# Kernel optimization log

Hardware: AMD Instinct MI355X
Metric: run time of the kernel (lower is better)

## Reference

```python
import jax, jax.numpy as jnp
import numpy as np

BETA = 0.1
TRUNC = 1.0
MIN_VALID_RATIO = 0.3


def _wls_affine(x, y, w):
    # Weighted least squares fit of y ~ s*x + t over the last axis.
    sw = w.sum(-1)
    swx = (w * x).sum(-1)
    swy = (w * y).sum(-1)
    swxx = (w * x * x).sum(-1)
    swxy = (w * x * y).sum(-1)
    det = sw * swxx - swx * swx
    det = jnp.where(jnp.abs(det) < 1e-12, 1e-12, det)
    s = (sw * swxy - swx * swy) / det
    t = (swxx * swy - swx * swxy) / det
    return s, t


def _align_depth_affine(x, y, w, trunc):
    # Truncated robust affine alignment: initial WLS fit, then refit with
    # weights of points whose weighted residual exceeds `trunc` zeroed out
    # (falling back to the original weights if everything is truncated).
    s0, t0 = _wls_affine(x, y, w)
    e = w * jnp.abs(s0[..., None] * x + t0[..., None] - y)
    w2 = w * (e < trunc).astype(w.dtype)
    w2 = jnp.where(w2.sum(-1, keepdims=True) > 1e-8, w2, w)
    return _wls_affine(x, y, w2)


def _smooth(err, beta):
    if beta == 0:
        return err
    return jnp.where(err < beta, 0.5 * err * err / beta, err - 0.5 * beta)


def setup_inputs() -> dict:
    key = jax.random.key(0)
    k1, k2, k3 = jax.random.split(key, 3)
    B = 8
    P = 4096  # num_patches
    K = 256   # patch_pixel_count
    N = P * K
    pred_depth = jax.random.uniform(k1, (B, N), jnp.float32, 0.05, 5.0)
    gt_depth = jax.random.uniform(k2, (B, N), jnp.float32, 0.05, 5.0)
    mask = jax.random.bernoulli(k3, 0.8, (B, N))
    global_scale = jnp.ones((B,), jnp.float32)
    return {
        "pred_depth": pred_depth,
        "gt_depth": gt_depth,
        "mask": mask,
        "global_scale": global_scale,
        "num_patches": P,
        "patch_pixel_count": K,
    }


def reference(pred_depth, gt_depth, mask, global_scale, num_patches, patch_pixel_count):
    B = pred_depth.shape[0]
    P, K = num_patches, patch_pixel_count
    x = pred_depth.reshape(B, P, K)
    y = gt_depth.reshape(B, P, K)
    m = mask.reshape(B, P, K).astype(x.dtype)

    valid_ratio = m.mean(-1)                      # (B, P)
    msum = m.sum(-1)
    mean_depth = jnp.where(msum > 0, (y * m).sum(-1) / jnp.maximum(msum, 1.0), 1.0)

    w = m / jnp.maximum(y, 1e-5)                  # alignment weights (B, P, K)
    s, t = _align_depth_affine(x, y, w, TRUNC)    # (B, P) scale / shift per patch

    ratio = s / jnp.maximum(global_scale[:, None], 1e-12)
    gs_ok = jnp.where(global_scale[:, None] > 0, (ratio >= 0.1) & (ratio <= 10.0), True)
    valid = (valid_ratio >= MIN_VALID_RATIO) & (s > 0) & gs_ok  # (B, P)

    aligned = s[..., None] * x + t[..., None]
    pw = m / jnp.maximum(y, 0.1 * mean_depth[..., None])
    patch_loss = _smooth(jnp.abs(aligned - y) * pw, BETA).mean(-1)  # (B, P)

    vf = valid.astype(x.dtype)
    cnt = vf.sum()
    loss = jnp.where(cnt > 0, (patch_loss * vf).sum() / jnp.maximum(cnt, 1.0), 0.0)
    return loss
```

## Files before the change

kernel.cpp:

```cpp
#include <hip/hip_runtime.h>


#define WPB 4
#define NSLOTS 64
#define MAXBLK 2048

__device__ __forceinline__ float wredu(float v) {
#define DPP_ADD(ctrl)                                                        \
  v += __int_as_float(__builtin_amdgcn_update_dpp(                           \
      0, __float_as_int(v), (ctrl), 0xf, 0xf, true))
  DPP_ADD(0x111);
  DPP_ADD(0x112);
  DPP_ADD(0x114);
  DPP_ADD(0x118);
  DPP_ADD(0x142);
  DPP_ADD(0x143);
#undef DPP_ADD
  return __int_as_float(__builtin_amdgcn_readlane(__float_as_int(v), 63));
}

__device__ __forceinline__ float frcp(float x) {
  return __builtin_amdgcn_rcpf(x);
}

__global__ __launch_bounds__(256) void moge_patch_kernel(
    const float* __restrict__ xg,
    const float* __restrict__ yg,
    const int*   __restrict__ mg,
    const float* __restrict__ gsg,
    const int*   __restrict__ pP,
    const int*   __restrict__ pK,
    int B,
    float* __restrict__ ws) {
  const int P = pP[0];
  const int K = pK[0];
  const int lane = threadIdx.x & 63;
  const int wib  = threadIdx.x >> 6;
  const int total_patches = B * P;
  const int wave_stride = gridDim.x * WPB;
  const float invK = 1.0f / (float)K;

  float wloss = 0.f, wcnt = 0.f;

  if (K == 256) {
    int patch = blockIdx.x * WPB + wib;
    if (patch < total_patches) {
      const int loff = lane * 4;
      long base = (long)patch * 256 + loff;
      float4 x4 = *(const float4*)(xg + base);
      float4 y4 = *(const float4*)(yg + base);
      int4   m4 = *(const int4*)(mg + base);

      for (;;) {
        const int next = patch + wave_stride;
        const bool has_next = next < total_patches;
        const long nbase = (has_next ? (long)next * 256 : 0) + loff;
        const float4 nx4 = *(const float4*)(xg + nbase);
        const float4 ny4 = *(const float4*)(yg + nbase);
        const int4   nm4 = *(const int4*)(mg + nbase);

        float xr[4] = {x4.x, x4.y, x4.z, x4.w};
        float yr[4] = {y4.x, y4.y, y4.z, y4.w};
        float mr[4] = {m4.x ? 1.f : 0.f, m4.y ? 1.f : 0.f,
                       m4.z ? 1.f : 0.f, m4.w ? 1.f : 0.f};
        float wr[4];

        float sw = 0.f, swx = 0.f, swy = 0.f, swxx = 0.f, swxy = 0.f;
        float msum = 0.f, symsum = 0.f;
        #pragma unroll
        for (int i = 0; i < 4; ++i) {
          const float m = mr[i], xx = xr[i], yy = yr[i];
          const float w = m * frcp(fmaxf(yy, 1e-5f));
          wr[i] = w;
          const float wx = w * xx;
          sw += w; swx += wx; swy = fmaf(w, yy, swy);
          swxx = fmaf(wx, xx, swxx); swxy = fmaf(wx, yy, swxy);
          msum += m; symsum = fmaf(m, yy, symsum);
        }
        sw = wredu(sw); swx = wredu(swx); swy = wredu(swy);
        swxx = wredu(swxx); swxy = wredu(swxy);

        float det = sw * swxx - swx * swx;
        if (fabsf(det) < 1e-12f) det = 1e-12f;
        float rdet = frcp(det);
        const float s0 = (sw * swxy - swx * swy) * rdet;
        const float t0 = (swxx * swy - swx * swxy) * rdet;

        float sw2 = 0.f, swx2 = 0.f, swy2 = 0.f, swxx2 = 0.f, swxy2 = 0.f;
        #pragma unroll
        for (int i = 0; i < 4; ++i) {
          const float xx = xr[i], yy = yr[i], w = wr[i];
          const float e = w * fabsf(fmaf(s0, xx, t0) - yy);
          const float w2 = (e < 1.0f) ? w : 0.f;
          const float w2x = w2 * xx;
          sw2 += w2; swx2 += w2x; swy2 = fmaf(w2, yy, swy2);
          swxx2 = fmaf(w2x, xx, swxx2); swxy2 = fmaf(w2x, yy, swxy2);
        }
        sw2 = wredu(sw2); swx2 = wredu(swx2); swy2 = wredu(swy2);
        swxx2 = wredu(swxx2); swxy2 = wredu(swxy2);
        msum = wredu(msum); symsum = wredu(symsum);

        if (sw2 > 1e-8f) {
          sw = sw2; swx = swx2; swy = swy2; swxx = swxx2; swxy = swxy2;
        }
        det = sw * swxx - swx * swx;
        if (fabsf(det) < 1e-12f) det = 1e-12f;
        rdet = frcp(det);
        const float s = (sw * swxy - swx * swy) * rdet;
        const float t = (swxx * swy - swx * swxy) * rdet;

        const float mean_depth =
            (msum > 0.f) ? (symsum * frcp(fmaxf(msum, 1.f))) : 1.f;
        const float yfloor = 0.1f * mean_depth;

        float lsum = 0.f;
        #pragma unroll
        for (int i = 0; i < 4; ++i) {
          const float pw = mr[i] * frcp(fmaxf(yr[i], yfloor));
          const float err = fabsf(fmaf(s, xr[i], t) - yr[i]) * pw;
          lsum += (err < 0.1f) ? (5.0f * err * err) : (err - 0.05f);
        }
        const float patch_loss = wredu(lsum) * invK;

        const float gs = gsg[patch / P];
        const float ratio = s * frcp(fmaxf(gs, 1e-12f));
        const bool gs_ok = (gs > 0.f) ? (ratio >= 0.1f && ratio <= 10.0f) : true;
        const bool valid = (msum * invK >= 0.3f) && (s > 0.f) && gs_ok;

        if (valid) { wloss += patch_loss; wcnt += 1.f; }

        if (!has_next) break;
        patch = next; x4 = nx4; y4 = ny4; m4 = nm4;
      }
    }
  } else {
    for (int patch = blockIdx.x * WPB + wib; patch < total_patches;
         patch += wave_stride) {
      const long base = (long)patch * (long)K;
      const float* xp = xg + base;
      const float* yp = yg + base;
      const int*   mp = mg + base;

      float sw = 0.f, swx = 0.f, swy = 0.f, swxx = 0.f, swxy = 0.f;
      float msum = 0.f, symsum = 0.f;
      for (int j = lane; j < K; j += 64) {
        const float m = mp[j] ? 1.f : 0.f;
        const float xx = xp[j], yy = yp[j];
        const float w = m * frcp(fmaxf(yy, 1e-5f));
        const float wx = w * xx;
        sw += w; swx += wx; swy = fmaf(w, yy, swy);
        swxx = fmaf(wx, xx, swxx); swxy = fmaf(wx, yy, swxy);
        msum += m; symsum = fmaf(m, yy, symsum);
      }
      sw = wredu(sw); swx = wredu(swx); swy = wredu(swy);
      swxx = wredu(swxx); swxy = wredu(swxy);
      msum = wredu(msum); symsum = wredu(symsum);

      float det = sw * swxx - swx * swx;
      if (fabsf(det) < 1e-12f) det = 1e-12f;
      float rdet = frcp(det);
      const float s0 = (sw * swxy - swx * swy) * rdet;
      const float t0 = (swxx * swy - swx * swxy) * rdet;

      float sw2 = 0.f, swx2 = 0.f, swy2 = 0.f, swxx2 = 0.f, swxy2 = 0.f;
      for (int j = lane; j < K; j += 64) {
        const float m = mp[j] ? 1.f : 0.f;
        const float xx = xp[j], yy = yp[j];
        const float w = m * frcp(fmaxf(yy, 1e-5f));
        const float e = w * fabsf(fmaf(s0, xx, t0) - yy);
        const float w2 = (e < 1.0f) ? w : 0.f;
        const float w2x = w2 * xx;
        sw2 += w2; swx2 += w2x; swy2 = fmaf(w2, yy, swy2);
        swxx2 = fmaf(w2x, xx, swxx2); swxy2 = fmaf(w2x, yy, swxy2);
      }
      sw2 = wredu(sw2); swx2 = wredu(swx2); swy2 = wredu(swy2);
      swxx2 = wredu(swxx2); swxy2 = wredu(swxy2);

      if (sw2 > 1e-8f) {
        sw = sw2; swx = swx2; swy = swy2; swxx = swxx2; swxy = swxy2;
      }
      det = sw * swxx - swx * swx;
      if (fabsf(det) < 1e-12f) det = 1e-12f;
      rdet = frcp(det);
      const float s = (sw * swxy - swx * swy) * rdet;
      const float t = (swxx * swy - swx * swxy) * rdet;

      const float mean_depth =
          (msum > 0.f) ? (symsum * frcp(fmaxf(msum, 1.f))) : 1.f;
      const float yfloor = 0.1f * mean_depth;

      float lsum = 0.f;
      for (int j = lane; j < K; j += 64) {
        const float m = mp[j] ? 1.f : 0.f;
        const float xx = xp[j], yy = yp[j];
        const float pw = m * frcp(fmaxf(yy, yfloor));
        const float err = fabsf(fmaf(s, xx, t) - yy) * pw;
        lsum += (err < 0.1f) ? (5.0f * err * err) : (err - 0.05f);
      }
      const float patch_loss = wredu(lsum) * invK;

      const float gs = gsg[patch / P];
      const float ratio = s * frcp(fmaxf(gs, 1e-12f));
      const bool gs_ok = (gs > 0.f) ? (ratio >= 0.1f && ratio <= 10.0f) : true;
      const bool valid = (msum * invK >= 0.3f) && (s > 0.f) && gs_ok;

      if (valid) { wloss += patch_loss; wcnt += 1.f; }
    }
  }

  __shared__ float sl[WPB], sc[WPB];
  if (lane == 0) { sl[wib] = wloss; sc[wib] = wcnt; }
  __syncthreads();
  if (threadIdx.x == 0) {
    float bl = 0.f, bc = 0.f;
    #pragma unroll
    for (int i = 0; i < WPB; ++i) { bl += sl[i]; bc += sc[i]; }
    const int slot = (blockIdx.x & (NSLOTS - 1)) * 32;
    atomicAdd(&ws[slot], bl);
    atomicAdd(&ws[slot + 1], bc);
  }
}

__global__ void finalize_kernel(const float* __restrict__ ws,
                                float* __restrict__ out) {
  const int t = threadIdx.x;
  float l = wredu(ws[t * 32]);
  float c = wredu(ws[t * 32 + 1]);
  if (t == 0) out[0] = (c > 0.f) ? (l / fmaxf(c, 1.f)) : 0.f;
}

extern "C" void kernel_launch(void* const* d_in, const int* in_sizes, int n_in,
                              void* d_out, int out_size, void* d_ws, size_t ws_size,
                              hipStream_t stream) {
  const float* pred = (const float*)d_in[0];
  const float* gt   = (const float*)d_in[1];
  const int*   mask = (const int*)d_in[2];
  const float* gs   = (const float*)d_in[3];
  const int*   pP   = (const int*)d_in[4];
  const int*   pK   = (const int*)d_in[5];
  const int B = in_sizes[3];
  const long total_pixels = (long)in_sizes[0];
  float* ws = (float*)d_ws;

  hipMemsetAsync(ws, 0, NSLOTS * 32 * sizeof(float), stream);

  long est_patches = total_pixels / 256;
  long blocks = (est_patches + WPB - 1) / WPB;
  if (blocks < 1) blocks = 1;
  if (blocks > MAXBLK) blocks = MAXBLK;
  moge_patch_kernel<<<(int)blocks, 256, 0, stream>>>(pred, gt, mask, gs, pP,
                                                     pK, B, ws);
  finalize_kernel<<<1, 64, 0, stream>>>(ws, (float*)d_out);
}
```

Measured before the change: 128.9 us.

## Process four patches per wave with 16-lane row reductions

Each wavefront now handles four patches at once: every 16-lane DPP row owns one patch and each lane loads 16 contiguous pixels as four float4 loads per array. Wave-wide reductions become 4-step row reductions, which cuts the cross-lane shuffle work per patch. The launch uses a quarter as many blocks. The explicit software prefetch of the next patch is removed, so latency hiding now relies on more loads in flight per lane and on occupancy, and register use goes up from the 16-element arrays.

Measured after the change: 127.9 us. No clear change (-0.7%).

```diff
diff --git a/kernel.cpp b/kernel.cpp
--- a/kernel.cpp
+++ b/kernel.cpp
@@ -2,6 +2,7 @@
 
 
 #define WPB 4
+#define PPW 4
 #define NSLOTS 64
 #define MAXBLK 2048
 
@@ -17,6 +18,18 @@
   DPP_ADD(0x143);
 #undef DPP_ADD
   return __int_as_float(__builtin_amdgcn_readlane(__float_as_int(v), 63));
+}
+
+__device__ __forceinline__ float rowredu(float v) {
+#define DPP_ADD(ctrl)                                                        \
+  v += __int_as_float(__builtin_amdgcn_update_dpp(                           \
+      0, __float_as_int(v), (ctrl), 0xf, 0xf, true))
+  DPP_ADD(0x121);
+  DPP_ADD(0x122);
+  DPP_ADD(0x124);
+  DPP_ADD(0x128);
+#undef DPP_ADD
+  return v;
 }
 
 __device__ __forceinline__ float frcp(float x) {
@@ -37,103 +50,103 @@
   const int lane = threadIdx.x & 63;
   const int wib  = threadIdx.x >> 6;
   const int total_patches = B * P;
-  const int wave_stride = gridDim.x * WPB;
   const float invK = 1.0f / (float)K;
 
   float wloss = 0.f, wcnt = 0.f;
 
   if (K == 256) {
-    int patch = blockIdx.x * WPB + wib;
-    if (patch < total_patches) {
-      const int loff = lane * 4;
-      long base = (long)patch * 256 + loff;
-      float4 x4 = *(const float4*)(xg + base);
-      float4 y4 = *(const float4*)(yg + base);
-      int4   m4 = *(const int4*)(mg + base);
-
-      for (;;) {
-        const int next = patch + wave_stride;
-        const bool has_next = next < total_patches;
-        const long nbase = (has_next ? (long)next * 256 : 0) + loff;
-        const float4 nx4 = *(const float4*)(xg + nbase);
-        const float4 ny4 = *(const float4*)(yg + nbase);
-        const int4   nm4 = *(const int4*)(mg + nbase);
-
-        float xr[4] = {x4.x, x4.y, x4.z, x4.w};
-        float yr[4] = {y4.x, y4.y, y4.z, y4.w};
-        float mr[4] = {m4.x ? 1.f : 0.f, m4.y ? 1.f : 0.f,
-                       m4.z ? 1.f : 0.f, m4.w ? 1.f : 0.f};
-        float wr[4];
-
-        float sw = 0.f, swx = 0.f, swy = 0.f, swxx = 0.f, swxy = 0.f;
-        float msum = 0.f, symsum = 0.f;
-        #pragma unroll
-        for (int i = 0; i < 4; ++i) {
-          const float m = mr[i], xx = xr[i], yy = yr[i];
-          const float w = m * frcp(fmaxf(yy, 1e-5f));
-          wr[i] = w;
-          const float wx = w * xx;
-          sw += w; swx += wx; swy = fmaf(w, yy, swy);
-          swxx = fmaf(wx, xx, swxx); swxy = fmaf(wx, yy, swxy);
-          msum += m; symsum = fmaf(m, yy, symsum);
-        }
-        sw = wredu(sw); swx = wredu(swx); swy = wredu(swy);
-        swxx = wredu(swxx); swxy = wredu(swxy);
-
-        float det = sw * swxx - swx * swx;
-        if (fabsf(det) < 1e-12f) det = 1e-12f;
-        float rdet = frcp(det);
-        const float s0 = (sw * swxy - swx * swy) * rdet;
-        const float t0 = (swxx * swy - swx * swxy) * rdet;
-
-        float sw2 = 0.f, swx2 = 0.f, swy2 = 0.f, swxx2 = 0.f, swxy2 = 0.f;
-        #pragma unroll
-        for (int i = 0; i < 4; ++i) {
-          const float xx = xr[i], yy = yr[i], w = wr[i];
-          const float e = w * fabsf(fmaf(s0, xx, t0) - yy);
-          const float w2 = (e < 1.0f) ? w : 0.f;
-          const float w2x = w2 * xx;
-          sw2 += w2; swx2 += w2x; swy2 = fmaf(w2, yy, swy2);
-          swxx2 = fmaf(w2x, xx, swxx2); swxy2 = fmaf(w2x, yy, swxy2);
-        }
-        sw2 = wredu(sw2); swx2 = wredu(swx2); swy2 = wredu(swy2);
-        swxx2 = wredu(swxx2); swxy2 = wredu(swxy2);
-        msum = wredu(msum); symsum = wredu(symsum);
-
-        if (sw2 > 1e-8f) {
-          sw = sw2; swx = swx2; swy = swy2; swxx = swxx2; swxy = swxy2;
-        }
-        det = sw * swxx - swx * swx;
-        if (fabsf(det) < 1e-12f) det = 1e-12f;
-        rdet = frcp(det);
-        const float s = (sw * swxy - swx * swy) * rdet;
-        const float t = (swxx * swy - swx * swxy) * rdet;
-
-        const float mean_depth =
-            (msum > 0.f) ? (symsum * frcp(fmaxf(msum, 1.f))) : 1.f;
-        const float yfloor = 0.1f * mean_depth;
-
-        float lsum = 0.f;
-        #pragma unroll
-        for (int i = 0; i < 4; ++i) {
-          const float pw = mr[i] * frcp(fmaxf(yr[i], yfloor));
-          const float err = fabsf(fmaf(s, xr[i], t) - yr[i]) * pw;
-          lsum += (err < 0.1f) ? (5.0f * err * err) : (err - 0.05f);
-        }
-        const float patch_loss = wredu(lsum) * invK;
-
-        const float gs = gsg[patch / P];
-        const float ratio = s * frcp(fmaxf(gs, 1e-12f));
-        const bool gs_ok = (gs > 0.f) ? (ratio >= 0.1f && ratio <= 10.0f) : true;
-        const bool valid = (msum * invK >= 0.3f) && (s > 0.f) && gs_ok;
-
-        if (valid) { wloss += patch_loss; wcnt += 1.f; }
-
-        if (!has_next) break;
-        patch = next; x4 = nx4; y4 = ny4; m4 = nm4;
-      }
+    const int row = lane >> 4;
+    const int col = lane & 15;
+    const int poff = col * 16;
+    const int wave_stride = gridDim.x * WPB * PPW;
+
+    for (int pbase = (blockIdx.x * WPB + wib) * PPW; pbase < total_patches;
+         pbase += wave_stride) {
+      const int patch = pbase + row;
+      const bool row_ok = patch < total_patches;
+      const long base = (row_ok ? (long)patch * 256L : 0L) + poff;
+
+      float4 xa[4], ya[4]; int4 ma[4];
+      #pragma unroll
+      for (int j = 0; j < 4; ++j) {
+        xa[j] = *(const float4*)(xg + base + 4 * j);
+        ya[j] = *(const float4*)(yg + base + 4 * j);
+        ma[j] = *(const int4*)(mg + base + 4 * j);
+      }
+      const float* xr = (const float*)xa;
+      const float* yr = (const float*)ya;
+      const int*   mi = (const int*)ma;
+      float wv[16];
+
+      float sw = 0.f, swx = 0.f, swy = 0.f, swxx = 0.f, swxy = 0.f;
+      float msum = 0.f, symsum = 0.f;
+      #pragma unroll
+      for (int i = 0; i < 16; ++i) {
+        const float m = mi[i] ? 1.f : 0.f;
+        const float xx = xr[i], yy = yr[i];
+        const float w = m * frcp(fmaxf(yy, 1e-5f));
+        wv[i] = w;
+        const float wx = w * xx;
+        sw += w; swx += wx; swy = fmaf(w, yy, swy);
+        swxx = fmaf(wx, xx, swxx); swxy = fmaf(wx, yy, swxy);
+        msum += m; symsum = fmaf(m, yy, symsum);
+      }
+      sw = rowredu(sw); swx = rowredu(swx); swy = rowredu(swy);
+      swxx = rowredu(swxx); swxy = rowredu(swxy);
+
+      float det = sw * swxx - swx * swx;
+      if (fabsf(det) < 1e-12f) det = 1e-12f;
+      float rdet = frcp(det);
+      const float s0 = (sw * swxy - swx * swy) * rdet;
+      const float t0 = (swxx * swy - swx * swxy) * rdet;
+
+      float sw2 = 0.f, swx2 = 0.f, swy2 = 0.f, swxx2 = 0.f, swxy2 = 0.f;
+      #pragma unroll
+      for (int i = 0; i < 16; ++i) {
+        const float xx = xr[i], yy = yr[i], w = wv[i];
+        const float e = w * fabsf(fmaf(s0, xx, t0) - yy);
+        const float w2 = (e < 1.0f) ? w : 0.f;
+        const float w2x = w2 * xx;
+        sw2 += w2; swx2 += w2x; swy2 = fmaf(w2, yy, swy2);
+        swxx2 = fmaf(w2x, xx, swxx2); swxy2 = fmaf(w2x, yy, swxy2);
+      }
+      sw2 = rowredu(sw2); swx2 = rowredu(swx2); swy2 = rowredu(swy2);
+      swxx2 = rowredu(swxx2); swxy2 = rowredu(swxy2);
+      msum = rowredu(msum); symsum = rowredu(symsum);
+
+      if (sw2 > 1e-8f) {
+        sw = sw2; swx = swx2; swy = swy2; swxx = swxx2; swxy = swxy2;
+      }
+      det = sw * swxx - swx * swx;
+      if (fabsf(det) < 1e-12f) det = 1e-12f;
+      rdet = frcp(det);
+      const float s = (sw * swxy - swx * swy) * rdet;
+      const float t = (swxx * swy - swx * swxy) * rdet;
+
+      const float mean_depth =
+          (msum > 0.f) ? (symsum * frcp(fmaxf(msum, 1.f))) : 1.f;
+      const float yfloor = 0.1f * mean_depth;
+
+      float lsum = 0.f;
+      #pragma unroll
+      for (int i = 0; i < 16; ++i) {
+        const float m = (wv[i] > 0.f) ? 1.f : 0.f;
+        const float pw = m * frcp(fmaxf(yr[i], yfloor));
+        const float err = fabsf(fmaf(s, xr[i], t) - yr[i]) * pw;
+        lsum += (err < 0.1f) ? (5.0f * err * err) : (err - 0.05f);
+      }
+      const float patch_loss = rowredu(lsum) * invK;
+
+      const int pidx = row_ok ? patch : (total_patches - 1);
+      const float gs = gsg[(unsigned)pidx / (unsigned)P];
+      const float ratio = s * frcp(fmaxf(gs, 1e-12f));
+      const bool gs_ok = (gs > 0.f) ? (ratio >= 0.1f && ratio <= 10.0f) : true;
+      const bool valid = (msum * invK >= 0.3f) && (s > 0.f) && gs_ok;
+
+      if (col == 0 && row_ok && valid) { wloss += patch_loss; wcnt += 1.f; }
     }
   } else {
+    const int wave_stride = gridDim.x * WPB;
     for (int patch = blockIdx.x * WPB + wib; patch < total_patches;
          patch += wave_stride) {
       const long base = (long)patch * (long)K;
@@ -199,15 +212,17 @@
       }
       const float patch_loss = wredu(lsum) * invK;
 
-      const float gs = gsg[patch / P];
+      const float gs = gsg[(unsigned)patch / (unsigned)P];
       const float ratio = s * frcp(fmaxf(gs, 1e-12f));
       const bool gs_ok = (gs > 0.f) ? (ratio >= 0.1f && ratio <= 10.0f) : true;
       const bool valid = (msum * invK >= 0.3f) && (s > 0.f) && gs_ok;
 
-      if (valid) { wloss += patch_loss; wcnt += 1.f; }
+      if (lane == 0 && valid) { wloss += patch_loss; wcnt += 1.f; }
     }
   }
 
+  wloss = wredu(wloss);
+  wcnt  = wredu(wcnt);
   __shared__ float sl[WPB], sc[WPB];
   if (lane == 0) { sl[wib] = wloss; sc[wib] = wcnt; }
   __syncthreads();
@@ -245,7 +260,7 @@
   hipMemsetAsync(ws, 0, NSLOTS * 32 * sizeof(float), stream);
 
   long est_patches = total_pixels / 256;
-  long blocks = (est_patches + WPB - 1) / WPB;
+  long blocks = (est_patches + WPB * PPW - 1) / (WPB * PPW);
   if (blocks < 1) blocks = 1;
   if (blocks > MAXBLK) blocks = MAXBLK;
   moge_patch_kernel<<<(int)blocks, 256, 0, stream>>>(pred, gt, mask, gs, pP,
```
